# Optimization experiments

Measured on AMD Instinct MI355X. Metric: run time of the kernel, lower is better.

The kernel has to match this reference:

```python
import jax, jax.numpy as jnp
import numpy as np

N = 100_000      # nodes
E = 1_600_000    # edges (avg degree 16)
EP = 500_000     # pos/neg decode edges each
IN, H, OUT = 256, 128, 64


def setup_inputs() -> dict:
    key = jax.random.key(0)
    ks = jax.random.split(key, 8)
    x = jax.random.normal(ks[0], (N, IN), dtype=jnp.float32)
    edge_index = jax.random.randint(ks[1], (2, E), 0, N, dtype=jnp.int32)
    pos_edge_index = jax.random.randint(ks[2], (2, EP), 0, N, dtype=jnp.int32)
    neg_edge_index = jax.random.randint(ks[3], (2, EP), 0, N, dtype=jnp.int32)
    W1 = jax.random.normal(ks[4], (IN, H), dtype=jnp.float32) * (1.0 / np.sqrt(IN))
    b1 = jnp.zeros((H,), dtype=jnp.float32)
    W2 = jax.random.normal(ks[5], (H, OUT), dtype=jnp.float32) * (1.0 / np.sqrt(H))
    b2 = jnp.zeros((OUT,), dtype=jnp.float32)
    return dict(x=x, edge_index=edge_index, pos_edge_index=pos_edge_index,
                neg_edge_index=neg_edge_index, W1=W1, b1=b1, W2=W2, b2=b2)


def _gcn_conv(x, src, dst, norm, W, b, n_nodes):
    # PyG GCNConv: linear transform, then normalized scatter-add aggregation
    h = x @ W                              # [N, out]
    msg = h[src] * norm[:, None]           # gather + scale, [E+N, out]
    agg = jax.ops.segment_sum(msg, dst, num_segments=n_nodes)
    return agg + b


def reference(x, edge_index, pos_edge_index, neg_edge_index, W1, b1, W2, b2):
    n = x.shape[0]
    loops = jnp.arange(n, dtype=edge_index.dtype)
    src = jnp.concatenate([edge_index[0], loops])   # add self-loops (GCNConv default)
    dst = jnp.concatenate([edge_index[1], loops])
    # symmetric normalization D^{-1/2} (A+I) D^{-1/2}
    deg = jax.ops.segment_sum(jnp.ones_like(src, dtype=x.dtype), dst, num_segments=n)
    dinv = jnp.where(deg > 0, jax.lax.rsqrt(jnp.maximum(deg, 1e-12)), 0.0)
    norm = dinv[src] * dinv[dst]
    # encode
    h = jax.nn.relu(_gcn_conv(x, src, dst, norm, W1, b1, n))
    z = _gcn_conv(h, src, dst, norm, W2, b2, n)
    # decode: edge score = <z_u, z_v> over pos+neg edges
    ei = jnp.concatenate([pos_edge_index, neg_edge_index], axis=-1)
    return (z[ei[0]] * z[ei[1]]).sum(axis=-1)   # [2*EP]
```

## Files before the change

### kernel.cpp

```cpp
#include <hip/hip_runtime.h>


typedef __attribute__((ext_vector_type(8))) short short8;
typedef __attribute__((ext_vector_type(4))) float f32x4;

#define BUK_SHIFT 7
#define BUK_NODES 128
#define CAP_SHIFT 12
#define BUK_CAP 4096

__global__ __launch_bounds__(256) void split_w_k(
    const float* __restrict__ W1, int K1, int N1, unsigned short* __restrict__ hi1,
    unsigned short* __restrict__ lo1, const float* __restrict__ W2, int K2, int N2,
    unsigned short* __restrict__ hi2, unsigned short* __restrict__ lo2,
    int* __restrict__ bcur, int nbuk) {
  int idx = blockIdx.x * 256 + threadIdx.x;
  if (idx < nbuk) bcur[idx] = 0;
  const int tot1 = K1 * N1;
  const float* W;
  unsigned short *hi, *lo;
  int K, N;
  if (idx < tot1) {
    W = W1; hi = hi1; lo = lo1; K = K1; N = N1;
  } else {
    idx -= tot1;
    if (idx >= K2 * N2) return;
    W = W2; hi = hi2; lo = lo2; K = K2; N = N2;
  }
  const int k = idx / N, c = idx - k * N;
  const float a = W[idx];
  const unsigned u = __float_as_uint(a);
  const unsigned short h = (unsigned short)(u >> 16);
  const float l = a - __uint_as_float(u & 0xFFFF0000u);
  const unsigned short lb = (unsigned short)(__float_as_uint(l) >> 16);
  hi[(size_t)c * K + k] = h;
  lo[(size_t)c * K + k] = lb;
}

__global__ __launch_bounds__(256) void b_scatter_k(const int* __restrict__ src,
                                                   const int* __restrict__ dst, int E,
                                                   int nbuk, int* __restrict__ bcur,
                                                   int* __restrict__ ebuf) {
  __shared__ int lh[1024];
  __shared__ int lc[1024];
  const int base = blockIdx.x * 8192;
  if (base >= E) return;
  const int end = min(base + 8192, E);
  for (int i = threadIdx.x; i < nbuk; i += 256) lh[i] = 0;
  __syncthreads();
  for (int i = base + threadIdx.x; i < end; i += 256)
    atomicAdd(&lh[dst[i] >> BUK_SHIFT], 1);
  __syncthreads();
  for (int i = threadIdx.x; i < nbuk; i += 256) {
    int c = lh[i];
    lc[i] = c ? (i << CAP_SHIFT) + atomicAdd(&bcur[i], c) : 0;
  }
  __syncthreads();
  for (int i = base + threadIdx.x; i < end; i += 256) {
    int d = dst[i];
    int pos = atomicAdd(&lc[d >> BUK_SHIFT], 1);
    ebuf[pos] = src[i] | ((d & (BUK_NODES - 1)) << 17);
  }
}

__global__ __launch_bounds__(128) void b_build_k(const int* __restrict__ ebuf,
                                                 const int* __restrict__ bcur, int n,
                                                 float* __restrict__ dinv,
                                                 int* __restrict__ rowbeg,
                                                 int* __restrict__ rowend,
                                                 int* __restrict__ csr) {
  __shared__ int cnt[BUK_NODES];
  __shared__ int pre[BUK_NODES];
  __shared__ int cur[BUK_NODES];
  const int b = blockIdx.x, t = threadIdx.x;
  cnt[t] = 0;
  __syncthreads();
  const int beg = b << CAP_SHIFT;
  const int end = beg + bcur[b];
  for (int i = beg + t; i < end; i += 128) atomicAdd(&cnt[ebuf[i] >> 17], 1);
  __syncthreads();
  const int c = cnt[t];
  pre[t] = c;
  __syncthreads();
  for (int off = 1; off < 128; off <<= 1) {
    int v = (t >= off) ? pre[t - off] : 0;
    __syncthreads();
    pre[t] += v;
    __syncthreads();
  }
  const int rb = beg + pre[t] - c;
  cur[t] = rb;
  const int node = (b << BUK_SHIFT) + t;
  if (node < n) {
    rowbeg[node] = rb;
    rowend[node] = rb + c;
    dinv[node] = rsqrtf((float)(c + 1));
  }
  __syncthreads();
  for (int i = beg + t; i < end; i += 128) {
    int e = ebuf[i];
    int pos = atomicAdd(&cur[e >> 17], 1);
    csr[pos] = e & 0x1FFFF;
  }
}

template <int BN>
__global__ __launch_bounds__(256) void gemm_mfma(
    const float* __restrict__ A, const unsigned short* __restrict__ Bthi,
    const unsigned short* __restrict__ Btlo, float* __restrict__ C,
    const float* __restrict__ rowscale, int M, int K) {
  constexpr int BM = 64, BK = 32;
  constexpr int NT = BN / 16;
  constexpr int LD = 40;
  __shared__ unsigned short Ahi[BM * LD];
  __shared__ unsigned short Alo[BM * LD];
  __shared__ unsigned short Bhi[BN * LD];
  __shared__ unsigned short Blo[BN * LD];
  const int tid = threadIdx.x;
  const int lane = tid & 63;
  const int wave = tid >> 6;
  const int rowBase = blockIdx.x * BM;

  f32x4 acc[NT];
#pragma unroll
  for (int c = 0; c < NT; ++c) acc[c] = (f32x4){0.f, 0.f, 0.f, 0.f};

  const int sr = tid >> 2;
  const int sk = (tid & 3) * 8;
  const int arow = wave * 16 + (lane & 15);
  const int akb = (lane >> 4) * 8;

  for (int k0 = 0; k0 < K; k0 += BK) {
    {
      const int gr = rowBase + sr;
      float4 v0 = make_float4(0.f, 0.f, 0.f, 0.f);
      float4 v1 = make_float4(0.f, 0.f, 0.f, 0.f);
      if (gr < M) {
        const float* p = A + (size_t)gr * K + k0 + sk;
        v0 = *reinterpret_cast<const float4*>(p);
        v1 = *reinterpret_cast<const float4*>(p + 4);
      }
      const float vv[8] = {v0.x, v0.y, v0.z, v0.w, v1.x, v1.y, v1.z, v1.w};
      short8 hv, lv;
#pragma unroll
      for (int i = 0; i < 8; ++i) {
        const unsigned u = __float_as_uint(vv[i]);
        hv[i] = (short)(u >> 16);
        const float l = vv[i] - __uint_as_float(u & 0xFFFF0000u);
        lv[i] = (short)(__float_as_uint(l) >> 16);
      }
      *reinterpret_cast<short8*>(&Ahi[sr * LD + sk]) = hv;
      *reinterpret_cast<short8*>(&Alo[sr * LD + sk]) = lv;
    }
    for (int i = tid; i < BN * 2; i += 256) {
      const int col = i >> 1;
      const int kk = (i & 1) * 16;
      const size_t gofs = (size_t)col * K + k0 + kk;
      *reinterpret_cast<short8*>(&Bhi[col * LD + kk]) =
          *reinterpret_cast<const short8*>(&Bthi[gofs]);
      *reinterpret_cast<short8*>(&Bhi[col * LD + kk + 8]) =
          *reinterpret_cast<const short8*>(&Bthi[gofs + 8]);
      *reinterpret_cast<short8*>(&Blo[col * LD + kk]) =
          *reinterpret_cast<const short8*>(&Btlo[gofs]);
      *reinterpret_cast<short8*>(&Blo[col * LD + kk + 8]) =
          *reinterpret_cast<const short8*>(&Btlo[gofs + 8]);
    }
    __syncthreads();
    const short8 fa_hi = *reinterpret_cast<const short8*>(&Ahi[arow * LD + akb]);
    const short8 fa_lo = *reinterpret_cast<const short8*>(&Alo[arow * LD + akb]);
#pragma unroll
    for (int c = 0; c < NT; ++c) {
      const int bofs = (c * 16 + (lane & 15)) * LD + akb;
      const short8 fb_hi = *reinterpret_cast<const short8*>(&Bhi[bofs]);
      const short8 fb_lo = *reinterpret_cast<const short8*>(&Blo[bofs]);
      acc[c] = __builtin_amdgcn_mfma_f32_16x16x32_bf16(fa_hi, fb_hi, acc[c], 0, 0, 0);
      acc[c] = __builtin_amdgcn_mfma_f32_16x16x32_bf16(fa_lo, fb_hi, acc[c], 0, 0, 0);
      acc[c] = __builtin_amdgcn_mfma_f32_16x16x32_bf16(fa_hi, fb_lo, acc[c], 0, 0, 0);
    }
    __syncthreads();
  }
  const int crow = rowBase + wave * 16 + (lane >> 4) * 4;
  float sc[4];
#pragma unroll
  for (int j = 0; j < 4; ++j) sc[j] = (crow + j < M) ? rowscale[crow + j] : 0.f;
#pragma unroll
  for (int c = 0; c < NT; ++c) {
#pragma unroll
    for (int j = 0; j < 4; ++j) {
      const int gr = crow + j;
      if (gr < M) C[(size_t)gr * BN + c * 16 + (lane & 15)] = acc[c][j] * sc[j];
    }
  }
}

__global__ __launch_bounds__(256) void agg128_gemm2_k(
    const float* __restrict__ g1, const int* __restrict__ rowbeg,
    const int* __restrict__ rowend, const int* __restrict__ csr,
    const float* __restrict__ dinv, const float* __restrict__ bias,
    const unsigned short* __restrict__ W2thi, const unsigned short* __restrict__ W2tlo,
    float* __restrict__ g2, int n) {
  constexpr int LD2 = 136;
  __shared__ unsigned short Hhi[32 * LD2];
  __shared__ unsigned short Hlo[32 * LD2];
  const int tid = threadIdx.x;
  const int lane = tid & 63;
  const int wave = tid >> 6;
  const int half = lane >> 5;
  const int nb = blockIdx.x * 32;

  const size_t col = (size_t)(lane & 31) * 4;
#pragma unroll
  for (int it = 0; it < 8; ++it) {
    const int row = wave * 8 + it;
    const int node = nb + row;
    float4 r = make_float4(0.f, 0.f, 0.f, 0.f);
    if (node < n) {
      const float dd = dinv[node];
      const int beg = rowbeg[node];
      const int end = rowend[node];
      float4 acc = make_float4(0.f, 0.f, 0.f, 0.f);
      int e = beg;
      for (; e + 8 <= end; e += 8) {
        const int s0 = csr[e + 0 + half];
        const int s1 = csr[e + 2 + half];
        const int s2 = csr[e + 4 + half];
        const int s3 = csr[e + 6 + half];
        const float4 v0 = *reinterpret_cast<const float4*>(&g1[(size_t)s0 * 128 + col]);
        const float4 v1 = *reinterpret_cast<const float4*>(&g1[(size_t)s1 * 128 + col]);
        const float4 v2 = *reinterpret_cast<const float4*>(&g1[(size_t)s2 * 128 + col]);
        const float4 v3 = *reinterpret_cast<const float4*>(&g1[(size_t)s3 * 128 + col]);
        acc.x += (v0.x + v1.x) + (v2.x + v3.x);
        acc.y += (v0.y + v1.y) + (v2.y + v3.y);
        acc.z += (v0.z + v1.z) + (v2.z + v3.z);
        acc.w += (v0.w + v1.w) + (v2.w + v3.w);
      }
      for (; e + 2 <= end; e += 2) {
        const int s = csr[e + half];
        const float4 v = *reinterpret_cast<const float4*>(&g1[(size_t)s * 128 + col]);
        acc.x += v.x;
        acc.y += v.y;
        acc.z += v.z;
        acc.w += v.w;
      }
      if (e < end && half == 0) {
        const int s = csr[e];
        const float4 v = *reinterpret_cast<const float4*>(&g1[(size_t)s * 128 + col]);
        acc.x += v.x;
        acc.y += v.y;
        acc.z += v.z;
        acc.w += v.w;
      }
      acc.x += __shfl_xor(acc.x, 32);
      acc.y += __shfl_xor(acc.y, 32);
      acc.z += __shfl_xor(acc.z, 32);
      acc.w += __shfl_xor(acc.w, 32);
      if (half == 0) {
        const float4 sv = *reinterpret_cast<const float4*>(&g1[(size_t)node * 128 + col]);
        const float4 b = *reinterpret_cast<const float4*>(&bias[col]);
        r.x = fmaxf(dd * (acc.x + sv.x) + b.x, 0.f);
        r.y = fmaxf(dd * (acc.y + sv.y) + b.y, 0.f);
        r.z = fmaxf(dd * (acc.z + sv.z) + b.z, 0.f);
        r.w = fmaxf(dd * (acc.w + sv.w) + b.w, 0.f);
      }
    }
    if (half == 0) {
      const float vv[4] = {r.x, r.y, r.z, r.w};
      ushort4 hv, lv;
      unsigned u0 = __float_as_uint(vv[0]);
      unsigned u1 = __float_as_uint(vv[1]);
      unsigned u2 = __float_as_uint(vv[2]);
      unsigned u3 = __float_as_uint(vv[3]);
      hv.x = (unsigned short)(u0 >> 16);
      hv.y = (unsigned short)(u1 >> 16);
      hv.z = (unsigned short)(u2 >> 16);
      hv.w = (unsigned short)(u3 >> 16);
      lv.x = (unsigned short)(__float_as_uint(vv[0] - __uint_as_float(u0 & 0xFFFF0000u)) >> 16);
      lv.y = (unsigned short)(__float_as_uint(vv[1] - __uint_as_float(u1 & 0xFFFF0000u)) >> 16);
      lv.z = (unsigned short)(__float_as_uint(vv[2] - __uint_as_float(u2 & 0xFFFF0000u)) >> 16);
      lv.w = (unsigned short)(__float_as_uint(vv[3] - __uint_as_float(u3 & 0xFFFF0000u)) >> 16);
      *reinterpret_cast<ushort4*>(&Hhi[row * LD2 + (lane & 31) * 4]) = hv;
      *reinterpret_cast<ushort4*>(&Hlo[row * LD2 + (lane & 31) * 4]) = lv;
    }
  }
  __syncthreads();

  const int ct = wave * 16;
  const int fr = lane & 15;
  const int fk = (lane >> 4) * 8;
  f32x4 acc2[2];
  acc2[0] = (f32x4){0.f, 0.f, 0.f, 0.f};
  acc2[1] = (f32x4){0.f, 0.f, 0.f, 0.f};
#pragma unroll
  for (int c = 0; c < 4; ++c) {
    const size_t bo = (size_t)(ct + fr) * 128 + c * 32 + fk;
    const short8 fb_hi = *reinterpret_cast<const short8*>(&W2thi[bo]);
    const short8 fb_lo = *reinterpret_cast<const short8*>(&W2tlo[bo]);
#pragma unroll
    for (int rt = 0; rt < 2; ++rt) {
      const short8 fa_hi =
          *reinterpret_cast<const short8*>(&Hhi[(rt * 16 + fr) * LD2 + c * 32 + fk]);
      const short8 fa_lo =
          *reinterpret_cast<const short8*>(&Hlo[(rt * 16 + fr) * LD2 + c * 32 + fk]);
      acc2[rt] = __builtin_amdgcn_mfma_f32_16x16x32_bf16(fa_hi, fb_hi, acc2[rt], 0, 0, 0);
      acc2[rt] = __builtin_amdgcn_mfma_f32_16x16x32_bf16(fa_lo, fb_hi, acc2[rt], 0, 0, 0);
      acc2[rt] = __builtin_amdgcn_mfma_f32_16x16x32_bf16(fa_hi, fb_lo, acc2[rt], 0, 0, 0);
    }
  }
#pragma unroll
  for (int rt = 0; rt < 2; ++rt) {
#pragma unroll
    for (int j = 0; j < 4; ++j) {
      const int node = nb + rt * 16 + (lane >> 4) * 4 + j;
      if (node < n) g2[(size_t)node * 64 + ct + fr] = acc2[rt][j] * dinv[node];
    }
  }
}

__global__ __launch_bounds__(256) void agg64_k(const float* __restrict__ g,
                                               const int* __restrict__ rowbeg,
                                               const int* __restrict__ rowend,
                                               const int* __restrict__ csr,
                                               const float* __restrict__ dinv,
                                               const float* __restrict__ bias,
                                               float* __restrict__ hout, int n) {
  const int wid = (blockIdx.x * 256 + threadIdx.x) >> 6;
  if (wid >= n) return;
  const int lane = threadIdx.x & 63;
  const int quad = lane >> 4;
  const size_t col = (size_t)(lane & 15) * 4;
  const float dd = dinv[wid];
  const int beg = rowbeg[wid];
  const int end = rowend[wid];
  float4 acc = make_float4(0.f, 0.f, 0.f, 0.f);
  int e = beg;
  for (; e + 16 <= end; e += 16) {
    const int s0 = csr[e + 0 + quad];
    const int s1 = csr[e + 4 + quad];
    const int s2 = csr[e + 8 + quad];
    const int s3 = csr[e + 12 + quad];
    const float4 v0 = *reinterpret_cast<const float4*>(&g[(size_t)s0 * 64 + col]);
    const float4 v1 = *reinterpret_cast<const float4*>(&g[(size_t)s1 * 64 + col]);
    const float4 v2 = *reinterpret_cast<const float4*>(&g[(size_t)s2 * 64 + col]);
    const float4 v3 = *reinterpret_cast<const float4*>(&g[(size_t)s3 * 64 + col]);
    acc.x += (v0.x + v1.x) + (v2.x + v3.x);
    acc.y += (v0.y + v1.y) + (v2.y + v3.y);
    acc.z += (v0.z + v1.z) + (v2.z + v3.z);
    acc.w += (v0.w + v1.w) + (v2.w + v3.w);
  }
  for (; e + 4 <= end; e += 4) {
    const int s = csr[e + quad];
    const float4 v = *reinterpret_cast<const float4*>(&g[(size_t)s * 64 + col]);
    acc.x += v.x;
    acc.y += v.y;
    acc.z += v.z;
    acc.w += v.w;
  }
  const int r = end - e;
  if (quad < r) {
    const int s = csr[e + quad];
    const float4 v = *reinterpret_cast<const float4*>(&g[(size_t)s * 64 + col]);
    acc.x += v.x;
    acc.y += v.y;
    acc.z += v.z;
    acc.w += v.w;
  }
  acc.x += __shfl_xor(acc.x, 16);
  acc.y += __shfl_xor(acc.y, 16);
  acc.z += __shfl_xor(acc.z, 16);
  acc.w += __shfl_xor(acc.w, 16);
  acc.x += __shfl_xor(acc.x, 32);
  acc.y += __shfl_xor(acc.y, 32);
  acc.z += __shfl_xor(acc.z, 32);
  acc.w += __shfl_xor(acc.w, 32);
  if (quad == 0) {
    const float4 sv = *reinterpret_cast<const float4*>(&g[(size_t)wid * 64 + col]);
    const float4 b = *reinterpret_cast<const float4*>(&bias[col]);
    float4 res;
    res.x = dd * (acc.x + sv.x) + b.x;
    res.y = dd * (acc.y + sv.y) + b.y;
    res.z = dd * (acc.z + sv.z) + b.z;
    res.w = dd * (acc.w + sv.w) + b.w;
    *reinterpret_cast<float4*>(&hout[(size_t)wid * 64 + col]) = res;
  }
}

__global__ __launch_bounds__(256) void decode_k(const int* __restrict__ pos,
                                                const int* __restrict__ neg,
                                                const float* __restrict__ z,
                                                float* __restrict__ out, int EP) {
  const long long t = (long long)blockIdx.x * 256 + threadIdx.x;
  const long long e = t >> 3;
  const int lane = (int)(t & 7);
  if (e >= 2LL * EP) return;
  int u, v;
  if (e < EP) {
    u = pos[e];
    v = pos[EP + e];
  } else {
    u = neg[e - EP];
    v = neg[EP + (e - EP)];
  }
  const float* zu = &z[(size_t)u * 64 + lane * 8];
  const float* zv = &z[(size_t)v * 64 + lane * 8];
  const float4 a0 = *reinterpret_cast<const float4*>(zu);
  const float4 a1 = *reinterpret_cast<const float4*>(zu + 4);
  const float4 b0 = *reinterpret_cast<const float4*>(zv);
  const float4 b1 = *reinterpret_cast<const float4*>(zv + 4);
  float p = a0.x * b0.x + a0.y * b0.y + a0.z * b0.z + a0.w * b0.w +
            a1.x * b1.x + a1.y * b1.y + a1.z * b1.z + a1.w * b1.w;
#pragma unroll
  for (int off = 4; off > 0; off >>= 1) p += __shfl_down(p, off, 8);
  if (lane == 0) out[e] = p;
}


extern "C" void kernel_launch(void* const* d_in, const int* in_sizes, int n_in,
                              void* d_out, int out_size, void* d_ws, size_t ws_size,
                              hipStream_t stream) {
  const float* x = (const float*)d_in[0];
  const int* ei = (const int*)d_in[1];
  const int* pos = (const int*)d_in[2];
  const int* neg = (const int*)d_in[3];
  const float* W1 = (const float*)d_in[4];
  const float* b1 = (const float*)d_in[5];
  const float* W2 = (const float*)d_in[6];
  const float* b2 = (const float*)d_in[7];
  float* out = (float*)d_out;

  const int H = in_sizes[5];
  const int IN = in_sizes[4] / H;
  const int OUT = in_sizes[7];
  const int N = in_sizes[0] / IN;
  const int E = in_sizes[1] / 2;
  const int EP = in_sizes[2] / 2;

  char* ws = (char*)d_ws;
  size_t off = 0;
  auto carve = [&](size_t bytes) -> char* {
    char* p = ws + off;
    off += (bytes + 255) & ~(size_t)255;
    return p;
  };
  const int NBUK = (N + BUK_NODES - 1) >> BUK_SHIFT;

  float* dinvb = (float*)carve((size_t)N * 4);
  int* rowbeg = (int*)carve((size_t)N * 4);
  int* rowend = (int*)carve((size_t)N * 4);
  int* bcur = (int*)carve((size_t)NBUK * 4);
  int* ebuf = (int*)carve((size_t)NBUK * BUK_CAP * 4);
  int* csr = (int*)carve((size_t)NBUK * BUK_CAP * 4);
  float* bufA = (float*)carve((size_t)N * H * 4);
  float* bufB = (float*)carve((size_t)N * H * 4);
  unsigned short* w1hi = (unsigned short*)carve((size_t)IN * H * 2);
  unsigned short* w1lo = (unsigned short*)carve((size_t)IN * H * 2);
  unsigned short* w2hi = (unsigned short*)carve((size_t)H * OUT * 2);
  unsigned short* w2lo = (unsigned short*)carve((size_t)H * OUT * 2);
  (void)ws_size;

  const int* srcp = ei;
  const int* dstp = ei + E;

  split_w_k<<<(IN * H + H * OUT + 255) / 256, 256, 0, stream>>>(
      W1, IN, H, w1hi, w1lo, W2, H, OUT, w2hi, w2lo, bcur, NBUK);
  b_scatter_k<<<(E + 8191) / 8192, 256, 0, stream>>>(srcp, dstp, E, NBUK, bcur, ebuf);
  b_build_k<<<NBUK, 128, 0, stream>>>(ebuf, bcur, N, dinvb, rowbeg, rowend, csr);
  gemm_mfma<128><<<(N + 63) / 64, 256, 0, stream>>>(x, w1hi, w1lo, bufA, dinvb, N, IN);
  agg128_gemm2_k<<<(N + 31) / 32, 256, 0, stream>>>(bufA, rowbeg, rowend, csr, dinvb,
                                                    b1, w2hi, w2lo, bufB, N);
  agg64_k<<<(N + 3) / 4, 256, 0, stream>>>(bufB, rowbeg, rowend, csr, dinvb, b2,
                                           bufA, N);
  const long long threads = 2LL * EP * 8;
  decode_k<<<(int)((threads + 255) / 256), 256, 0, stream>>>(pos, neg, bufA, out, EP);
}
```

Baseline: 349.6 us.

## Merge CSR build into GEMM1 launch via global degree atomics; widen decode lanes

Node degrees are now counted with global atomics during the bucket scatter, so GEMM1 no longer depends on the CSR build. The two are merged into one launch in which the first blocks build the CSR and the remaining blocks run the MFMA GEMM concurrently, and dinv is recomputed from the degree where it is needed. The decode kernel uses 4 lanes per edge with 16 floats each instead of 8 lanes with 8. This removes a launch and a serial dependency, at the cost of 1.6M global atomics and extra rsqrt work in the later kernels.

```diff
diff --git a/kernel.cpp b/kernel.cpp
--- a/kernel.cpp
+++ b/kernel.cpp
@@ -13,9 +13,10 @@
     const float* __restrict__ W1, int K1, int N1, unsigned short* __restrict__ hi1,
     unsigned short* __restrict__ lo1, const float* __restrict__ W2, int K2, int N2,
     unsigned short* __restrict__ hi2, unsigned short* __restrict__ lo2,
-    int* __restrict__ bcur, int nbuk) {
+    int* __restrict__ bcur, int nbuk, int* __restrict__ deg, int n) {
   int idx = blockIdx.x * 256 + threadIdx.x;
   if (idx < nbuk) bcur[idx] = 0;
+  if (idx < n) deg[idx] = 0;
   const int tot1 = K1 * N1;
   const float* W;
   unsigned short *hi, *lo;
@@ -40,7 +41,8 @@
 __global__ __launch_bounds__(256) void b_scatter_k(const int* __restrict__ src,
                                                    const int* __restrict__ dst, int E,
                                                    int nbuk, int* __restrict__ bcur,
-                                                   int* __restrict__ ebuf) {
+                                                   int* __restrict__ ebuf,
+                                                   int* __restrict__ deg) {
   __shared__ int lh[1024];
   __shared__ int lc[1024];
   const int base = blockIdx.x * 8192;
@@ -48,8 +50,11 @@
   const int end = min(base + 8192, E);
   for (int i = threadIdx.x; i < nbuk; i += 256) lh[i] = 0;
   __syncthreads();
-  for (int i = base + threadIdx.x; i < end; i += 256)
-    atomicAdd(&lh[dst[i] >> BUK_SHIFT], 1);
+  for (int i = base + threadIdx.x; i < end; i += 256) {
+    const int d = dst[i];
+    atomicAdd(&lh[d >> BUK_SHIFT], 1);
+    atomicAdd(&deg[d], 1);
+  }
   __syncthreads();
   for (int i = threadIdx.x; i < nbuk; i += 256) {
     int c = lh[i];
@@ -63,63 +68,64 @@
   }
 }
 
-__global__ __launch_bounds__(128) void b_build_k(const int* __restrict__ ebuf,
-                                                 const int* __restrict__ bcur, int n,
-                                                 float* __restrict__ dinv,
-                                                 int* __restrict__ rowbeg,
-                                                 int* __restrict__ rowend,
-                                                 int* __restrict__ csr) {
-  __shared__ int cnt[BUK_NODES];
-  __shared__ int pre[BUK_NODES];
-  __shared__ int cur[BUK_NODES];
-  const int b = blockIdx.x, t = threadIdx.x;
-  cnt[t] = 0;
-  __syncthreads();
-  const int beg = b << CAP_SHIFT;
-  const int end = beg + bcur[b];
-  for (int i = beg + t; i < end; i += 128) atomicAdd(&cnt[ebuf[i] >> 17], 1);
-  __syncthreads();
-  const int c = cnt[t];
-  pre[t] = c;
-  __syncthreads();
-  for (int off = 1; off < 128; off <<= 1) {
-    int v = (t >= off) ? pre[t - off] : 0;
-    __syncthreads();
-    pre[t] += v;
-    __syncthreads();
-  }
-  const int rb = beg + pre[t] - c;
-  cur[t] = rb;
-  const int node = (b << BUK_SHIFT) + t;
-  if (node < n) {
-    rowbeg[node] = rb;
-    rowend[node] = rb + c;
-    dinv[node] = rsqrtf((float)(c + 1));
-  }
-  __syncthreads();
-  for (int i = beg + t; i < end; i += 128) {
-    int e = ebuf[i];
-    int pos = atomicAdd(&cur[e >> 17], 1);
-    csr[pos] = e & 0x1FFFF;
-  }
-}
-
-template <int BN>
-__global__ __launch_bounds__(256) void gemm_mfma(
-    const float* __restrict__ A, const unsigned short* __restrict__ Bthi,
+__global__ __launch_bounds__(256) void build_gemm1_k(
+    const int* __restrict__ ebuf, const int* __restrict__ bcur, int n, int nbuk,
+    int* __restrict__ rowbeg, int* __restrict__ rowend, int* __restrict__ csr,
+    const float* __restrict__ X, const unsigned short* __restrict__ Bthi,
     const unsigned short* __restrict__ Btlo, float* __restrict__ C,
-    const float* __restrict__ rowscale, int M, int K) {
-  constexpr int BM = 64, BK = 32;
-  constexpr int NT = BN / 16;
-  constexpr int LD = 40;
-  __shared__ unsigned short Ahi[BM * LD];
-  __shared__ unsigned short Alo[BM * LD];
-  __shared__ unsigned short Bhi[BN * LD];
-  __shared__ unsigned short Blo[BN * LD];
+    const int* __restrict__ deg, int M, int K) {
+  __shared__ unsigned short smem[15360];
   const int tid = threadIdx.x;
+
+  if ((int)blockIdx.x < nbuk) {
+    int* cnt = (int*)smem;
+    int* pre = cnt + BUK_NODES;
+    int* cur = pre + BUK_NODES;
+    const int b = blockIdx.x;
+    if (tid < BUK_NODES) cnt[tid] = 0;
+    __syncthreads();
+    const int beg = b << CAP_SHIFT;
+    const int end = beg + bcur[b];
+    for (int i = beg + tid; i < end; i += 256) atomicAdd(&cnt[ebuf[i] >> 17], 1);
+    __syncthreads();
+    int c = 0;
+    if (tid < BUK_NODES) {
+      c = cnt[tid];
+      pre[tid] = c;
+    }
+    __syncthreads();
+    for (int off = 1; off < BUK_NODES; off <<= 1) {
+      int v = (tid < BUK_NODES && tid >= off) ? pre[tid - off] : 0;
+      __syncthreads();
+      if (tid < BUK_NODES) pre[tid] += v;
+      __syncthreads();
+    }
+    if (tid < BUK_NODES) {
+      const int rb = beg + pre[tid] - c;
+      cur[tid] = rb;
+      const int node = (b << BUK_SHIFT) + tid;
+      if (node < n) {
+        rowbeg[node] = rb;
+        rowend[node] = rb + c;
+      }
+    }
+    __syncthreads();
+    for (int i = beg + tid; i < end; i += 256) {
+      int e = ebuf[i];
+      int pos = atomicAdd(&cur[e >> 17], 1);
+      csr[pos] = e & 0x1FFFF;
+    }
+    return;
+  }
+
+  constexpr int BM = 64, BN = 128, BK = 32, NT = BN / 16, LD = 40;
+  unsigned short* Ahi = smem;
+  unsigned short* Alo = Ahi + BM * LD;
+  unsigned short* Bhi = Alo + BM * LD;
+  unsigned short* Blo = Bhi + BN * LD;
   const int lane = tid & 63;
   const int wave = tid >> 6;
-  const int rowBase = blockIdx.x * BM;
+  const int rowBase = ((int)blockIdx.x - nbuk) * BM;
 
   f32x4 acc[NT];
 #pragma unroll
@@ -136,7 +142,7 @@
       float4 v0 = make_float4(0.f, 0.f, 0.f, 0.f);
       float4 v1 = make_float4(0.f, 0.f, 0.f, 0.f);
       if (gr < M) {
-        const float* p = A + (size_t)gr * K + k0 + sk;
+        const float* p = X + (size_t)gr * K + k0 + sk;
         v0 = *reinterpret_cast<const float4*>(p);
         v1 = *reinterpret_cast<const float4*>(p + 4);
       }
@@ -182,7 +188,8 @@
   const int crow = rowBase + wave * 16 + (lane >> 4) * 4;
   float sc[4];
 #pragma unroll
-  for (int j = 0; j < 4; ++j) sc[j] = (crow + j < M) ? rowscale[crow + j] : 0.f;
+  for (int j = 0; j < 4; ++j)
+    sc[j] = (crow + j < M) ? rsqrtf((float)(deg[crow + j] + 1)) : 0.f;
 #pragma unroll
   for (int c = 0; c < NT; ++c) {
 #pragma unroll
@@ -196,7 +203,7 @@
 __global__ __launch_bounds__(256) void agg128_gemm2_k(
     const float* __restrict__ g1, const int* __restrict__ rowbeg,
     const int* __restrict__ rowend, const int* __restrict__ csr,
-    const float* __restrict__ dinv, const float* __restrict__ bias,
+    const int* __restrict__ deg, const float* __restrict__ bias,
     const unsigned short* __restrict__ W2thi, const unsigned short* __restrict__ W2tlo,
     float* __restrict__ g2, int n) {
   constexpr int LD2 = 136;
@@ -215,7 +222,7 @@
     const int node = nb + row;
     float4 r = make_float4(0.f, 0.f, 0.f, 0.f);
     if (node < n) {
-      const float dd = dinv[node];
+      const float dd = rsqrtf((float)(deg[node] + 1));
       const int beg = rowbeg[node];
       const int end = rowend[node];
       float4 acc = make_float4(0.f, 0.f, 0.f, 0.f);
@@ -311,7 +318,9 @@
 #pragma unroll
     for (int j = 0; j < 4; ++j) {
       const int node = nb + rt * 16 + (lane >> 4) * 4 + j;
-      if (node < n) g2[(size_t)node * 64 + ct + fr] = acc2[rt][j] * dinv[node];
+      if (node < n)
+        g2[(size_t)node * 64 + ct + fr] =
+            acc2[rt][j] * rsqrtf((float)(deg[node] + 1));
     }
   }
 }
@@ -320,7 +329,7 @@
                                                const int* __restrict__ rowbeg,
                                                const int* __restrict__ rowend,
                                                const int* __restrict__ csr,
-                                               const float* __restrict__ dinv,
+                                               const int* __restrict__ deg,
                                                const float* __restrict__ bias,
                                                float* __restrict__ hout, int n) {
   const int wid = (blockIdx.x * 256 + threadIdx.x) >> 6;
@@ -328,7 +337,7 @@
   const int lane = threadIdx.x & 63;
   const int quad = lane >> 4;
   const size_t col = (size_t)(lane & 15) * 4;
-  const float dd = dinv[wid];
+  const float dd = rsqrtf((float)(deg[wid] + 1));
   const int beg = rowbeg[wid];
   const int end = rowend[wid];
   float4 acc = make_float4(0.f, 0.f, 0.f, 0.f);
@@ -389,8 +398,8 @@
                                                 const float* __restrict__ z,
                                                 float* __restrict__ out, int EP) {
   const long long t = (long long)blockIdx.x * 256 + threadIdx.x;
-  const long long e = t >> 3;
-  const int lane = (int)(t & 7);
+  const long long e = t >> 2;
+  const int lane = (int)(t & 3);
   if (e >= 2LL * EP) return;
   int u, v;
   if (e < EP) {
@@ -400,16 +409,22 @@
     u = neg[e - EP];
     v = neg[EP + (e - EP)];
   }
-  const float* zu = &z[(size_t)u * 64 + lane * 8];
-  const float* zv = &z[(size_t)v * 64 + lane * 8];
+  const float* zu = &z[(size_t)u * 64 + lane * 16];
+  const float* zv = &z[(size_t)v * 64 + lane * 16];
   const float4 a0 = *reinterpret_cast<const float4*>(zu);
   const float4 a1 = *reinterpret_cast<const float4*>(zu + 4);
+  const float4 a2 = *reinterpret_cast<const float4*>(zu + 8);
+  const float4 a3 = *reinterpret_cast<const float4*>(zu + 12);
   const float4 b0 = *reinterpret_cast<const float4*>(zv);
   const float4 b1 = *reinterpret_cast<const float4*>(zv + 4);
-  float p = a0.x * b0.x + a0.y * b0.y + a0.z * b0.z + a0.w * b0.w +
-            a1.x * b1.x + a1.y * b1.y + a1.z * b1.z + a1.w * b1.w;
-#pragma unroll
-  for (int off = 4; off > 0; off >>= 1) p += __shfl_down(p, off, 8);
+  const float4 b2 = *reinterpret_cast<const float4*>(zv + 8);
+  const float4 b3 = *reinterpret_cast<const float4*>(zv + 12);
+  float p = a0.x * b0.x + a0.y * b0.y + a0.z * b0.z + a0.w * b0.w;
+  p += a1.x * b1.x + a1.y * b1.y + a1.z * b1.z + a1.w * b1.w;
+  p += a2.x * b2.x + a2.y * b2.y + a2.z * b2.z + a2.w * b2.w;
+  p += a3.x * b3.x + a3.y * b3.y + a3.z * b3.z + a3.w * b3.w;
+  p += __shfl_down(p, 2, 4);
+  p += __shfl_down(p, 1, 4);
   if (lane == 0) out[e] = p;
 }
 
@@ -443,7 +458,7 @@
   };
   const int NBUK = (N + BUK_NODES - 1) >> BUK_SHIFT;
 
-  float* dinvb = (float*)carve((size_t)N * 4);
+  int* deg = (int*)carve((size_t)N * 4);
   int* rowbeg = (int*)carve((size_t)N * 4);
   int* rowend = (int*)carve((size_t)N * 4);
   int* bcur = (int*)carve((size_t)NBUK * 4);
@@ -460,15 +475,19 @@
   const int* srcp = ei;
   const int* dstp = ei + E;
 
-  split_w_k<<<(IN * H + H * OUT + 255) / 256, 256, 0, stream>>>(
-      W1, IN, H, w1hi, w1lo, W2, H, OUT, w2hi, w2lo, bcur, NBUK);
-  b_scatter_k<<<(E + 8191) / 8192, 256, 0, stream>>>(srcp, dstp, E, NBUK, bcur, ebuf);
-  b_build_k<<<NBUK, 128, 0, stream>>>(ebuf, bcur, N, dinvb, rowbeg, rowend, csr);
-  gemm_mfma<128><<<(N + 63) / 64, 256, 0, stream>>>(x, w1hi, w1lo, bufA, dinvb, N, IN);
-  agg128_gemm2_k<<<(N + 31) / 32, 256, 0, stream>>>(bufA, rowbeg, rowend, csr, dinvb,
+  const int splitThreads = IN * H + H * OUT;
+  const int initBlocks = (max(splitThreads, max(N, NBUK)) + 255) / 256;
+  split_w_k<<<initBlocks, 256, 0, stream>>>(W1, IN, H, w1hi, w1lo, W2, H, OUT, w2hi,
+                                            w2lo, bcur, NBUK, deg, N);
+  b_scatter_k<<<(E + 8191) / 8192, 256, 0, stream>>>(srcp, dstp, E, NBUK, bcur, ebuf,
+                                                     deg);
+  const int GB = (N + 63) / 64;
+  build_gemm1_k<<<NBUK + GB, 256, 0, stream>>>(ebuf, bcur, N, NBUK, rowbeg, rowend,
+                                               csr, x, w1hi, w1lo, bufA, deg, N, IN);
+  agg128_gemm2_k<<<(N + 31) / 32, 256, 0, stream>>>(bufA, rowbeg, rowend, csr, deg,
                                                     b1, w2hi, w2lo, bufB, N);
-  agg64_k<<<(N + 3) / 4, 256, 0, stream>>>(bufB, rowbeg, rowend, csr, dinvb, b2,
-                                           bufA, N);
-  const long long threads = 2LL * EP * 8;
+  agg64_k<<<(N + 3) / 4, 256, 0, stream>>>(bufB, rowbeg, rowend, csr, deg, b2, bufA,
+                                           N);
+  const long long threads = 2LL * EP * 4;
   decode_k<<<(int)((threads + 255) / 256), 256, 0, stream>>>(pos, neg, bufA, out, EP);
 }
```

Result: slower. 390.2 us (+11.6%).
